# Kernel tuning notes

Hardware: AMD Instinct MI355X
Metric: run time of the kernel (lower is better)

Reference implementation:

```python
import jax, jax.numpy as jnp
import numpy as np

B, T, F = 256, 512, 64
H1, H2, OUT = 100, 128, 19


def setup_inputs() -> dict:
    key = jax.random.key(0)
    ks = jax.random.split(key, 6)
    s = 0.05  # small init so relu cell activation stays stable over 512 steps
    return {
        "x":  jax.random.normal(ks[0], (B, T, F), jnp.float32),
        "W1": jax.random.normal(ks[1], (F, 4 * H1), jnp.float32) * s,
        "U1": jax.random.normal(ks[2], (H1, 4 * H1), jnp.float32) * s,
        "b1": jnp.zeros((4 * H1,), jnp.float32),
        "W2": jax.random.normal(ks[3], (H1, 4 * H2), jnp.float32) * s,
        "U2": jax.random.normal(ks[4], (H2, 4 * H2), jnp.float32) * s,
        "b2": jnp.zeros((4 * H2,), jnp.float32),
        "Wd": jax.random.normal(ks[5], (H2, OUT), jnp.float32) * s,
        "bd": jnp.zeros((OUT,), jnp.float32),
    }


def _lstm_relu(x, W, U, b):
    """Keras LSTM with activation=relu, recurrent_activation=sigmoid.
    x: [B,T,F]. Returns full hidden sequence [B,T,H]. Gate order i,f,g,o."""
    H = U.shape[0]
    xproj = jnp.einsum('btf,fj->btj', x, W) + b  # [B,T,4H], input gemm hoisted out of scan

    def step(carry, xt):
        h, c = carry
        z = xt + h @ U                            # [B,4H]
        i, f, g, o = jnp.split(z, 4, axis=-1)
        i = jax.nn.sigmoid(i)
        f = jax.nn.sigmoid(f)
        g = jax.nn.relu(g)
        o = jax.nn.sigmoid(o)
        c = f * c + i * g
        h = o * jax.nn.relu(c)
        return (h, c), h

    h0 = jnp.zeros((x.shape[0], H), x.dtype)
    c0 = jnp.zeros_like(h0)
    _, hs = jax.lax.scan(step, (h0, c0), jnp.swapaxes(xproj, 0, 1))  # [T,B,H]
    return jnp.swapaxes(hs, 0, 1)


def reference(x, W1, U1, b1, W2, U2, b2, Wd, bd):
    h1 = _lstm_relu(x, W1, U1, b1)    # [B,T,H1] (return_sequences=True, stacked intent)
    h2 = _lstm_relu(h1, W2, U2, b2)   # [B,T,H2]
    last = h2[:, -1]                   # [B,H2] last timestep
    return jax.nn.softmax(last @ Wd + bd, axis=-1)
```

## Files before the change

### kernel.cpp

```cpp
#include <hip/hip_runtime.h>
#include <math.h>

#define B_   256
#define T_   512
#define F_   64
#define H1_  100
#define H2_  128
#define OUT_ 19
#define TCH  64
#define NCH  (T_/TCH)
#define NPC  512
#define KP   128

typedef unsigned int uint;
typedef _Float16 h16;
typedef __attribute__((ext_vector_type(2))) _Float16 h16x2;
typedef __attribute__((ext_vector_type(8))) _Float16 f16x8;
typedef __attribute__((ext_vector_type(4))) float f32x4;

#define XPW_BYTES (16ull*TCH*NPC*16*2)
#define H1G_BYTES (16ull*TCH*KP*16*2)
#define CST_BYTES (16ull*KP*16*4)
#define HST_BYTES (16ull*KP*16*2)
#define UF_BYTES  (128ull*64*8*2)

#define A_XP1A  0ull
#define A_XP1B  (A_XP1A + XPW_BYTES)
#define A_XP2A  (A_XP1B + XPW_BYTES)
#define A_XP2B  (A_XP2A + XPW_BYTES)
#define A_H1GA  (A_XP2B + XPW_BYTES)
#define A_H1GB  (A_H1GA + H1G_BYTES)
#define A_C1    (A_H1GB + H1G_BYTES)
#define A_C2    (A_C1   + CST_BYTES)
#define A_H1S   (A_C2   + CST_BYTES)
#define A_H2S   (A_H1S  + HST_BYTES)
#define A_U1F   (A_H2S  + HST_BYTES)
#define A_U2F   (A_U1F  + UF_BYTES)
#define A_W1F   (A_U2F  + UF_BYTES)
#define A_W2F   (A_W1F  + UF_BYTES)
#define WS_A    (A_W2F  + UF_BYTES)

__device__ __forceinline__ float sigm(float x) { return 1.0f / (1.0f + __expf(-x)); }

__device__ __forceinline__ uint pk2(float a, float b) {
    h16x2 h; h.x = (h16)a; h.y = (h16)b;
    return __builtin_bit_cast(uint, h);
}

__device__ __forceinline__ f32x4 mfma16(f16x8 a, f16x8 b, f32x4 c) {
    return __builtin_amdgcn_mfma_f32_16x16x32_f16(a, b, c, 0, 0, 0);
}

__device__ __forceinline__ f32x4 up4(uint2 v) {
    h16x2 a = __builtin_bit_cast(h16x2, v.x);
    h16x2 b = __builtin_bit_cast(h16x2, v.y);
    f32x4 r; r[0] = (float)a.x; r[1] = (float)a.y; r[2] = (float)b.x; r[3] = (float)b.y;
    return r;
}

__device__ __forceinline__ void bar_lgkm() {
    asm volatile("s_waitcnt lgkmcnt(0)" ::: "memory");
    __builtin_amdgcn_sched_barrier(0);
    __builtin_amdgcn_s_barrier();
    __builtin_amdgcn_sched_barrier(0);
}

__device__ __forceinline__ f16x8 load_bfrag(const float* __restrict__ P, int H, int OG,
                                            int Kreal, int ubase, int g, int q, int lane) {
    const int u  = ubase + (lane & 15);
    const int k0 = q * 32 + (lane >> 4) * 8;
    const int col = g * H + u;
    float f[8];
    #pragma unroll
    for (int e = 0; e < 8; ++e) {
        const int k = k0 + e;
        f[e] = (u < H && k < Kreal) ? P[(size_t)k * OG + col] : 0.0f;
    }
    uint4 r;
    r.x = pk2(f[0], f[1]); r.y = pk2(f[2], f[3]);
    r.z = pk2(f[4], f[5]); r.w = pk2(f[6], f[7]);
    return __builtin_bit_cast(f16x8, r);
}

__global__ __launch_bounds__(512) void k_prepack4(
    const float* __restrict__ U1, const float* __restrict__ U2,
    const float* __restrict__ W1, const float* __restrict__ W2,
    h16* __restrict__ u1f, h16* __restrict__ u2f,
    h16* __restrict__ w1f, h16* __restrict__ w2f)
{
    const int w = blockIdx.x & 7;
    const int which = blockIdx.x >> 3;
    const float* P; int H, K, KF; h16* D;
    if (which == 0)      { P = U1; H = H1_; K = H1_; KF = 4; D = u1f; }
    else if (which == 1) { P = U2; H = H2_; K = H2_; KF = 4; D = u2f; }
    else if (which == 2) { P = W1; H = H1_; K = 64;  KF = 2; D = w1f; }
    else                 { P = W2; H = H2_; K = H1_; KF = 4; D = w2f; }
    const int lane = threadIdx.x & 63;
    #pragma unroll
    for (int it = 0; it < 2; ++it) {
        const int combo = it * 8 + (threadIdx.x >> 6);
        const int g = combo >> 2, q = combo & 3;
        if (q < KF) {
            f16x8 fr = load_bfrag(P, H, 4 * H, K, w * 16, g, q, lane);
            *(f16x8*)(D + (size_t)(((w * 4 + g) * 4 + q) * 64 + lane) * 8) = fr;
        }
    }
}

template<int MODE, int NIT>
__device__ __forceinline__ void dense_body(
    const float* __restrict__ Af, const h16* __restrict__ Ah,
    const h16* __restrict__ Wf, const float* __restrict__ bias,
    const int H, const int ch, h16* __restrict__ xp,
    const int bid, const int j)
{
    const int lane = j & 63, w = j >> 6;
    const int KF = MODE ? 4 : 2;

    f16x8 bf[4][4];
    #pragma unroll
    for (int g = 0; g < 4; ++g)
        #pragma unroll
        for (int q = 0; q < 4; ++q)
            if (q < KF)
                bf[g][q] = *(const f16x8*)(Wf + (size_t)(((w * 4 + g) * 4 + q) * 64 + lane) * 8);

    float bv[4];
    #pragma unroll
    for (int g = 0; g < 4; ++g) {
        const int u = w * 16 + (lane & 15);
        bv[g] = (u < H) ? bias[g * H + u] : 0.0f;
    }

    const int ci = lane & 15, hi = lane >> 4;
    #pragma unroll
    for (int it = 0; it < NIT; ++it) {
        const int m = bid * NIT + it;
        const int bt = m / TCH, tc = m % TCH;

        f16x8 af[4];
        if (MODE == 0) {
            const int b = bt * 16 + ci;
            const int t = ch * TCH + tc;
            #pragma unroll
            for (int q = 0; q < 2; ++q) {
                const int k0 = q * 32 + hi * 8;
                const float* p = Af + ((size_t)b * T_ + t) * F_ + k0;
                float4 x0 = *(const float4*)p;
                float4 x1 = *(const float4*)(p + 4);
                uint4 r;
                r.x = pk2(x0.x, x0.y); r.y = pk2(x0.z, x0.w);
                r.z = pk2(x1.x, x1.y); r.w = pk2(x1.z, x1.w);
                af[q] = __builtin_bit_cast(f16x8, r);
            }
        } else {
            #pragma unroll
            for (int q = 0; q < 4; ++q) {
                const int k0 = q * 32 + hi * 8;
                const size_t base = ((size_t)(bt * TCH + tc) * KP + k0) * 16 + ci;
                f16x8 a;
                #pragma unroll
                for (int e = 0; e < 8; ++e) a[e] = Ah[base + (size_t)e * 16];
                af[q] = a;
            }
        }

        f32x4 acc[4];
        #pragma unroll
        for (int g = 0; g < 4; ++g) { acc[g][0]=bv[g]; acc[g][1]=bv[g]; acc[g][2]=bv[g]; acc[g][3]=bv[g]; }
        #pragma unroll
        for (int g = 0; g < 4; ++g)
            #pragma unroll
            for (int q = 0; q < 4; ++q)
                if (q < KF) acc[g] = mfma16(af[q], bf[g][q], acc[g]);

        #pragma unroll
        for (int g = 0; g < 4; ++g) {
            const int c = (w * 4 + g) * 16 + ci;
            const size_t o = ((size_t)(bt * TCH + tc) * NPC + c) * 16 + hi * 4;
            uint2 s;
            s.x = pk2(acc[g][0], acc[g][1]);
            s.y = pk2(acc[g][2], acc[g][3]);
            *(uint2*)(xp + o) = s;
        }
    }
}

template<int MODE>
__global__ __launch_bounds__(512) void k_dense(
    const float* __restrict__ Af, const h16* __restrict__ Ah,
    const h16* __restrict__ Wf, const float* __restrict__ bias,
    const int H, const int ch, h16* __restrict__ xp)
{
    dense_body<MODE, 4>(Af, Ah, Wf, bias, H, ch, xp, blockIdx.x, threadIdx.x);
}

#define LF(G,Q) f16x8 wf##G##Q = *(const f16x8*)(Uf + (size_t)(((w*4+G)*4+Q)*64 + lane)*8);

#define RSTEP(Pn, tcur)                                                          \
    {                                                                            \
        const int t_ = (tcur);                                                   \
        const h16* hb = &hbuf[t_ & 1][0][0];                                     \
        f16x8 a0 = *(const f16x8*)(hb + ci * 136 + 0  + hi * 8);                 \
        f16x8 a1 = *(const f16x8*)(hb + ci * 136 + 32 + hi * 8);                 \
        f16x8 a2 = *(const f16x8*)(hb + ci * 136 + 64 + hi * 8);                 \
        f16x8 a3 = *(const f16x8*)(hb + ci * 136 + 96 + hi * 8);                 \
        f32x4 z0 = up4(Pn##0), z1 = up4(Pn##1), z2 = up4(Pn##2), z3 = up4(Pn##3);\
        const uint to_ = (uint)((t_ + 2 < TCH) ? t_ + 2 : t_) * xstep;           \
        Pn##0 = *(const uint2*)(xp + xb0 + to_);                                 \
        Pn##1 = *(const uint2*)(xp + xb1 + to_);                                 \
        Pn##2 = *(const uint2*)(xp + xb2 + to_);                                 \
        Pn##3 = *(const uint2*)(xp + xb3 + to_);                                 \
        z0 = mfma16(a0, wf00, z0); z0 = mfma16(a1, wf01, z0);                    \
        z0 = mfma16(a2, wf02, z0); z0 = mfma16(a3, wf03, z0);                    \
        z1 = mfma16(a0, wf10, z1); z1 = mfma16(a1, wf11, z1);                    \
        z1 = mfma16(a2, wf12, z1); z1 = mfma16(a3, wf13, z1);                    \
        z2 = mfma16(a0, wf20, z2); z2 = mfma16(a1, wf21, z2);                    \
        z2 = mfma16(a2, wf22, z2); z2 = mfma16(a3, wf23, z2);                    \
        z3 = mfma16(a0, wf30, z3); z3 = mfma16(a1, wf31, z3);                    \
        z3 = mfma16(a2, wf32, z3); z3 = mfma16(a3, wf33, z3);                    \
        f32x4 hv;                                                                \
        _Pragma("unroll")                                                        \
        for (int i = 0; i < 4; ++i) {                                            \
            float ig = sigm(z0[i]);                                              \
            float fg = sigm(z1[i]);                                              \
            float gg = fmaxf(z2[i], 0.0f);                                       \
            float og = sigm(z3[i]);                                              \
            c[i] = fg * c[i] + ig * gg;                                          \
            hv[i] = og * fmaxf(c[i], 0.0f);                                      \
        }                                                                        \
        h16 h0 = (h16)hv[0], h1 = (h16)hv[1], h2 = (h16)hv[2], h3 = (h16)hv[3]; \
        const int nb_ = (t_ & 1) ^ 1;                                            \
        hbuf[nb_][r0 + 0][myu] = h0;                                             \
        hbuf[nb_][r0 + 1][myu] = h1;                                             \
        hbuf[nb_][r0 + 2][myu] = h2;                                             \
        hbuf[nb_][r0 + 3][myu] = h3;                                             \
        h16x2 p01_; p01_.x = h0; p01_.y = h1;                                    \
        h16x2 p23_; p23_.x = h2; p23_.y = h3;                                    \
        hp.x = __builtin_bit_cast(uint, p01_);                                   \
        hp.y = __builtin_bit_cast(uint, p23_);                                   \
        if (do_hout) *(uint2*)(hout + hob + (uint)t_ * hstep) = hp;              \
        bar_lgkm();                                                              \
    }

__device__ __forceinline__ void rec_body(
    const h16* __restrict__ Uf,
    const h16* __restrict__ xp, h16* __restrict__ hout, const int do_hout,
    float* __restrict__ cstate, h16* __restrict__ hstate, const int ch,
    const int bt, const int j)
{
    __shared__ h16 hbuf[2][16][136];
    const int lane = j & 63, w = j >> 6;
    const int ci = lane & 15, hi = lane >> 4;
    const int myu = w * 16 + ci;
    const int r0 = hi * 4;

    LF(0,0) LF(0,1) LF(0,2) LF(0,3)
    LF(1,0) LF(1,1) LF(1,2) LF(1,3)
    LF(2,0) LF(2,1) LF(2,2) LF(2,3)
    LF(3,0) LF(3,1) LF(3,2) LF(3,3)

    {
        const int u = j & 127, rr = (j >> 7) * 4;
        #pragma unroll
        for (int i = 0; i < 4; ++i) {
            h16 v = (h16)0.0f;
            if (ch != 0) v = hstate[((size_t)bt * KP + u) * 16 + rr + i];
            hbuf[0][rr + i][u] = v;
        }
    }
    f32x4 c;
    const size_t coff = ((size_t)bt * KP + myu) * 16 + r0;
    if (ch == 0) { c[0]=0.f; c[1]=0.f; c[2]=0.f; c[3]=0.f; }
    else         { c = *(const f32x4*)(cstate + coff); }
    __syncthreads();

    const uint xstep = NPC * 16;
    const uint xb0 = (uint)(((size_t)bt * TCH) * NPC + (w * 64 + ci)) * 16 + r0;
    const uint xb1 = xb0 + 16 * 16, xb2 = xb0 + 32 * 16, xb3 = xb0 + 48 * 16;

    uint2 pA0 = *(const uint2*)(xp + xb0);
    uint2 pA1 = *(const uint2*)(xp + xb1);
    uint2 pA2 = *(const uint2*)(xp + xb2);
    uint2 pA3 = *(const uint2*)(xp + xb3);
    uint2 pB0 = *(const uint2*)(xp + xb0 + xstep);
    uint2 pB1 = *(const uint2*)(xp + xb1 + xstep);
    uint2 pB2 = *(const uint2*)(xp + xb2 + xstep);
    uint2 pB3 = *(const uint2*)(xp + xb3 + xstep);

    const uint hstep = KP * 16;
    const uint hob = (uint)(((size_t)bt * TCH) * KP + myu) * 16 + r0;

    uint2 hp; hp.x = 0u; hp.y = 0u;

    for (int tt = 0; tt < TCH; tt += 2) {
        RSTEP(pA, tt)
        RSTEP(pB, tt + 1)
    }

    *(f32x4*)(cstate + coff) = c;
    *(uint2*)(hstate + ((size_t)bt * KP + myu) * 16 + r0) = hp;
}

__global__ __launch_bounds__(512) void k_mega(
    const int rec2_on, const h16* __restrict__ Uf2, const h16* __restrict__ xp2r,
    float* __restrict__ c2, h16* __restrict__ hs2, const int ch2,
    const int rec1_on, const h16* __restrict__ Uf1, const h16* __restrict__ xp1r,
    h16* __restrict__ h1gw, float* __restrict__ c1, h16* __restrict__ hs1, const int ch1,
    const int d2_on, const h16* __restrict__ h1gr, const h16* __restrict__ w2f,
    const float* __restrict__ b2, h16* __restrict__ xp2w,
    const int d1_on, const float* __restrict__ x, const h16* __restrict__ w1f,
    const float* __restrict__ b1, const int chd1, h16* __restrict__ xp1w)
{
    const int bid = blockIdx.x, j = threadIdx.x;
    if (bid < 16) {
        if (rec2_on) rec_body(Uf2, xp2r, (h16*)nullptr, 0, c2, hs2, ch2, bid, j);
    } else if (bid < 32) {
        if (rec1_on) rec_body(Uf1, xp1r, h1gw, 1, c1, hs1, ch1, bid - 16, j);
    } else if (bid < 288) {
        if (d2_on) dense_body<1, 4>((const float*)nullptr, h1gr, w2f, b2, H2_, 0, xp2w, bid - 32, j);
    } else {
        if (d1_on) dense_body<0, 4>(x, (const h16*)nullptr, w1f, b1, H1_, chd1, xp1w, bid - 288, j);
    }
}

__global__ void k_head(const h16* __restrict__ h2s, const float* __restrict__ Wd,
                       const float* __restrict__ bd, float* __restrict__ out)
{
    __shared__ float lg[OUT_];
    const int b = blockIdx.x, j = threadIdx.x;
    const int bt = b >> 4, r = b & 15;
    if (j < OUT_) {
        float acc = bd[j];
        for (int u = 0; u < H2_; ++u)
            acc += (float)h2s[((size_t)bt * KP + u) * 16 + r] * Wd[u * OUT_ + j];
        lg[j] = acc;
    }
    __syncthreads();
    if (j < OUT_) {
        float m = -1e30f;
        for (int k = 0; k < OUT_; ++k) m = fmaxf(m, lg[k]);
        float s = 0.0f;
        for (int k = 0; k < OUT_; ++k) s += expf(lg[k] - m);
        out[b * OUT_ + j] = expf(lg[j] - m) / s;
    }
}

#define G1_  400
#define G2_  512
#define FBTC 32
#define FB_XP1  0
#define FB_XP2  0
#define FB_WQ   51200
#define FB_XS   134400
#define FB_W2Q  32768
#define FB_H1C  139264
#define FB_U2Q  32768
#define FB_ZBUF 160000
#define FB_H1PK 162048
#define FB_H2PK 162256
#define FB_H2F  162512
#define FB_LDS  163328

__device__ __forceinline__ float fd2(uint wv, uint hv, float cc) {
#if __has_builtin(__builtin_amdgcn_fdot2)
    return __builtin_amdgcn_fdot2(__builtin_bit_cast(h16x2, wv),
                                  __builtin_bit_cast(h16x2, hv), cc, false);
#else
    h16x2 a = __builtin_bit_cast(h16x2, wv), b = __builtin_bit_cast(h16x2, hv);
    return cc + (float)a.x * (float)b.x + (float)a.y * (float)b.y;
#endif
}

__device__ __forceinline__ void stage_quads(const float* __restrict__ P, const int G,
                                            const int NQ, const int KREAL,
                                            char* dst, const int j)
{
    if (j < G) {
        for (int q = 0; q < NQ; ++q) {
            float f[8];
            #pragma unroll
            for (int r = 0; r < 8; ++r) {
                const int k = 8 * q + r;
                f[r] = (k < KREAL) ? P[(size_t)k * G + j] : 0.0f;
            }
            uint4 u;
            u.x = pk2(f[0], f[1]); u.y = pk2(f[2], f[3]);
            u.z = pk2(f[4], f[5]); u.w = pk2(f[6], f[7]);
            *(uint4*)(dst + (size_t)(q * G + j) * 16) = u;
        }
    }
}

__global__ __launch_bounds__(512) void lstm_fallback(
    const float* __restrict__ x,
    const float* __restrict__ W1, const float* __restrict__ U1, const float* __restrict__ b1,
    const float* __restrict__ W2, const float* __restrict__ U2, const float* __restrict__ b2,
    const float* __restrict__ Wd, const float* __restrict__ bd,
    float* __restrict__ out)
{
    __shared__ uint4 smem4[FB_LDS / 16];
    char* sm = (char*)smem4;
    const int b = blockIdx.x;
    const int j = threadIdx.x;
    float c1 = 0.0f, c2 = 0.0f;

    const uint u2r0 = pk2(U2[120 * G2_ + j], U2[121 * G2_ + j]);
    const uint u2r1 = pk2(U2[122 * G2_ + j], U2[123 * G2_ + j]);
    const uint u2r2 = pk2(U2[124 * G2_ + j], U2[125 * G2_ + j]);
    const uint u2r3 = pk2(U2[126 * G2_ + j], U2[127 * G2_ + j]);

    if (j < 52) *(uint*)(sm + FB_H1PK + 4 * j) = 0u;
    if (j < 64) *(uint*)(sm + FB_H2PK + 4 * j) = 0u;
    __syncthreads();

    const float* xrow = x + (size_t)b * T_ * F_;
    for (int ch = 0; ch < T_ / FBTC; ++ch) {
        stage_quads(W1, G1_, 8, 64, sm + FB_WQ, j);
        #pragma unroll
        for (int r = 0; r < 2; ++r) {
            int v = r * 512 + j;
            float2 xv = *(const float2*)(xrow + ch * (FBTC * F_) + 2 * v);
            *(uint*)(sm + FB_XS + 4 * v) = pk2(xv.x, xv.y);
        }
        __syncthreads();
        if (j < G1_) {
            const float bj = b1[j];
            const uint4* WQ = (const uint4*)(sm + FB_WQ);
            for (int t = 0; t < FBTC; ++t) {
                const uint4* XQ = (const uint4*)(sm + FB_XS + t * 128);
                float a0 = bj, a1 = 0.f, a2 = 0.f, a3 = 0.f;
                #pragma unroll
                for (int q = 0; q < 8; ++q) {
                    uint4 wq = WQ[q * G1_ + j]; uint4 hq = XQ[q];
                    a0 = fd2(wq.x, hq.x, a0); a1 = fd2(wq.y, hq.y, a1);
                    a2 = fd2(wq.z, hq.z, a2); a3 = fd2(wq.w, hq.w, a3);
                }
                *(float*)(sm + FB_XP1 + 4 * (t * G1_ + j)) = (a0 + a1) + (a2 + a3);
            }
        }
        __syncthreads();
        stage_quads(U1, G1_, 13, H1_, sm + FB_WQ, j);
        __syncthreads();
        for (int t = 0; t < FBTC; ++t) {
            if (j < G1_) {
                const uint4* WQ = (const uint4*)(sm + FB_WQ);
                const uint4* HP = (const uint4*)(sm + FB_H1PK);
                float a0 = *(const float*)(sm + FB_XP1 + 4 * (t * G1_ + j));
                float a1 = 0.f, a2 = 0.f, a3 = 0.f;
                #pragma unroll
                for (int q = 0; q < 13; ++q) {
                    uint4 wq = WQ[q * G1_ + j]; uint4 hq = HP[q];
                    a0 = fd2(wq.x, hq.x, a0); a1 = fd2(wq.y, hq.y, a1);
                    a2 = fd2(wq.z, hq.z, a2); a3 = fd2(wq.w, hq.w, a3);
                }
                *(float*)(sm + FB_ZBUF + 4 * j) = (a0 + a1) + (a2 + a3);
            }
            __syncthreads();
            if (j < H1_) {
                const float* zb = (const float*)(sm + FB_ZBUF);
                float ig = sigm(zb[j]);
                float fg = sigm(zb[H1_ + j]);
                float gg = fmaxf(zb[2 * H1_ + j], 0.0f);
                float og = sigm(zb[3 * H1_ + j]);
                c1 = fg * c1 + ig * gg;
                float h = og * fmaxf(c1, 0.0f);
                h16 hh = (h16)h;
                *(h16*)(sm + FB_H1PK + 2 * j) = hh;
                *(h16*)(sm + FB_H1C + t * 208 + 2 * j) = hh;
            }
            __syncthreads();
        }
        stage_quads(W2, G2_, 13, H1_, sm + FB_W2Q, j);
        __syncthreads();
        {
            const float bj = b2[j];
            const uint4* WQ = (const uint4*)(sm + FB_W2Q);
            for (int t = 0; t < FBTC; ++t) {
                const uint4* HC = (const uint4*)(sm + FB_H1C + t * 208);
                float a0 = bj, a1 = 0.f, a2 = 0.f, a3 = 0.f;
                #pragma unroll
                for (int q = 0; q < 13; ++q) {
                    uint4 wq = WQ[q * G2_ + j]; uint4 hq = HC[q];
                    a0 = fd2(wq.x, hq.x, a0); a1 = fd2(wq.y, hq.y, a1);
                    a2 = fd2(wq.z, hq.z, a2); a3 = fd2(wq.w, hq.w, a3);
                }
                *(h16*)(sm + FB_XP2 + 2 * (t * G2_ + j)) = (h16)((a0 + a1) + (a2 + a3));
            }
        }
        __syncthreads();
        stage_quads(U2, G2_, 15, 120, sm + FB_U2Q, j);
        __syncthreads();
        for (int t = 0; t < FBTC; ++t) {
            {
                const uint4* WQ = (const uint4*)(sm + FB_U2Q);
                const uint4* HP = (const uint4*)(sm + FB_H2PK);
                float a0 = (float)*(const h16*)(sm + FB_XP2 + 2 * (t * G2_ + j));
                float a1 = 0.f, a2 = 0.f, a3 = 0.f;
                #pragma unroll
                for (int q = 0; q < 15; ++q) {
                    uint4 wq = WQ[q * G2_ + j]; uint4 hq = HP[q];
                    a0 = fd2(wq.x, hq.x, a0); a1 = fd2(wq.y, hq.y, a1);
                    a2 = fd2(wq.z, hq.z, a2); a3 = fd2(wq.w, hq.w, a3);
                }
                uint4 hp15 = ((const uint4*)(sm + FB_H2PK))[15];
                a0 = fd2(u2r0, hp15.x, a0); a1 = fd2(u2r1, hp15.y, a1);
                a2 = fd2(u2r2, hp15.z, a2); a3 = fd2(u2r3, hp15.w, a3);
                *(float*)(sm + FB_ZBUF + 4 * j) = (a0 + a1) + (a2 + a3);
            }
            __syncthreads();
            if (j < H2_) {
                const float* zb = (const float*)(sm + FB_ZBUF);
                float ig = sigm(zb[j]);
                float fg = sigm(zb[H2_ + j]);
                float gg = fmaxf(zb[2 * H2_ + j], 0.0f);
                float og = sigm(zb[3 * H2_ + j]);
                c2 = fg * c2 + ig * gg;
                float h = og * fmaxf(c2, 0.0f);
                *(h16*)(sm + FB_H2PK + 2 * j) = (h16)h;
                *(float*)(sm + FB_H2F + 4 * j) = h;
            }
            __syncthreads();
        }
    }
    if (j < OUT_) {
        const float* h2 = (const float*)(sm + FB_H2F);
        float acc = bd[j];
        #pragma unroll
        for (int k = 0; k < H2_; ++k) acc += h2[k] * Wd[k * OUT_ + j];
        *(float*)(sm + FB_ZBUF + 4 * j) = acc;
    }
    __syncthreads();
    if (j < OUT_) {
        const float* zb = (const float*)(sm + FB_ZBUF);
        float m = -1e30f;
        for (int k = 0; k < OUT_; ++k) m = fmaxf(m, zb[k]);
        float s = 0.0f;
        for (int k = 0; k < OUT_; ++k) s += expf(zb[k] - m);
        out[b * OUT_ + j] = expf(zb[j] - m) / s;
    }
}

extern "C" void kernel_launch(void* const* d_in, const int* in_sizes, int n_in,
                              void* d_out, int out_size, void* d_ws, size_t ws_size,
                              hipStream_t stream) {
    const float* x  = (const float*)d_in[0];
    const float* W1 = (const float*)d_in[1];
    const float* U1 = (const float*)d_in[2];
    const float* b1 = (const float*)d_in[3];
    const float* W2 = (const float*)d_in[4];
    const float* U2 = (const float*)d_in[5];
    const float* b2 = (const float*)d_in[6];
    const float* Wd = (const float*)d_in[7];
    const float* bd = (const float*)d_in[8];
    float* out = (float*)d_out;

    if (ws_size >= WS_A) {
        char* ws = (char*)d_ws;
        h16* xp1[2] = { (h16*)(ws + A_XP1A), (h16*)(ws + A_XP1B) };
        h16* xp2[2] = { (h16*)(ws + A_XP2A), (h16*)(ws + A_XP2B) };
        h16* h1g[2] = { (h16*)(ws + A_H1GA), (h16*)(ws + A_H1GB) };
        float* c1  = (float*)(ws + A_C1);
        float* c2  = (float*)(ws + A_C2);
        h16*   hs1 = (h16*)(ws + A_H1S);
        h16*   hs2 = (h16*)(ws + A_H2S);
        h16*   u1f = (h16*)(ws + A_U1F);
        h16*   u2f = (h16*)(ws + A_U2F);
        h16*   w1f = (h16*)(ws + A_W1F);
        h16*   w2f = (h16*)(ws + A_W2F);

        k_prepack4<<<32, 512, 0, stream>>>(U1, U2, W1, W2, u1f, u2f, w1f, w2f);
        k_dense<0><<<256, 512, 0, stream>>>(x, (const h16*)nullptr, w1f, b1, H1_, 0, xp1[0]);
        k_mega<<<544, 512, 0, stream>>>(
            0, u2f, (const h16*)nullptr, c2, hs2, 0,
            1, u1f, xp1[0], h1g[0], c1, hs1, 0,
            0, (const h16*)nullptr, w2f, b2, (h16*)nullptr,
            1, x, w1f, b1, 1, xp1[1]);
        k_mega<<<544, 512, 0, stream>>>(
            0, u2f, (const h16*)nullptr, c2, hs2, 0,
            1, u1f, xp1[1], h1g[1], c1, hs1, 1,
            1, h1g[0], w2f, b2, xp2[0],
            1, x, w1f, b1, 2, xp1[0]);
        for (int ch = 0; ch < NCH; ++ch) {
            const int r1on = (ch + 2 < NCH);
            const int d2on = (ch + 1 < NCH);
            const int d1on = (ch + 3 < NCH);
            k_mega<<<544, 512, 0, stream>>>(
                1, u2f, xp2[ch & 1], c2, hs2, ch,
                r1on, u1f, xp1[(ch + 2) & 1], h1g[(ch + 2) & 1], c1, hs1, ch + 2,
                d2on, h1g[(ch + 1) & 1], w2f, b2, xp2[(ch + 1) & 1],
                d1on, x, w1f, b1, ch + 3, xp1[(ch + 3) & 1]);
        }
        k_head<<<256, 64, 0, stream>>>(hs2, Wd, bd, out);
    } else {
        lstm_fallback<<<B_, 512, 0, stream>>>(x, W1, U1, b1, W2, U2, b2, Wd, bd, out);
    }
}
```

Baseline: 777.4 us.

## Halve time chunk size and fuse weight prepack with first dense projection

```diff
diff --git a/kernel.cpp b/kernel.cpp
--- a/kernel.cpp
+++ b/kernel.cpp
@@ -7,7 +7,7 @@
 #define H1_  100
 #define H2_  128
 #define OUT_ 19
-#define TCH  64
+#define TCH  32
 #define NCH  (T_/TCH)
 #define NPC  512
 #define KP   128
@@ -82,56 +82,21 @@
     return __builtin_bit_cast(f16x8, r);
 }
 
-__global__ __launch_bounds__(512) void k_prepack4(
-    const float* __restrict__ U1, const float* __restrict__ U2,
-    const float* __restrict__ W1, const float* __restrict__ W2,
-    h16* __restrict__ u1f, h16* __restrict__ u2f,
-    h16* __restrict__ w1f, h16* __restrict__ w2f)
-{
-    const int w = blockIdx.x & 7;
-    const int which = blockIdx.x >> 3;
-    const float* P; int H, K, KF; h16* D;
-    if (which == 0)      { P = U1; H = H1_; K = H1_; KF = 4; D = u1f; }
-    else if (which == 1) { P = U2; H = H2_; K = H2_; KF = 4; D = u2f; }
-    else if (which == 2) { P = W1; H = H1_; K = 64;  KF = 2; D = w1f; }
-    else                 { P = W2; H = H2_; K = H1_; KF = 4; D = w2f; }
-    const int lane = threadIdx.x & 63;
-    #pragma unroll
-    for (int it = 0; it < 2; ++it) {
-        const int combo = it * 8 + (threadIdx.x >> 6);
-        const int g = combo >> 2, q = combo & 3;
-        if (q < KF) {
-            f16x8 fr = load_bfrag(P, H, 4 * H, K, w * 16, g, q, lane);
-            *(f16x8*)(D + (size_t)(((w * 4 + g) * 4 + q) * 64 + lane) * 8) = fr;
-        }
-    }
-}
-
 template<int MODE, int NIT>
-__device__ __forceinline__ void dense_body(
+__device__ __forceinline__ void dense_core(
     const float* __restrict__ Af, const h16* __restrict__ Ah,
-    const h16* __restrict__ Wf, const float* __restrict__ bias,
+    const f16x8 bf[4][4], const float* __restrict__ bias,
     const int H, const int ch, h16* __restrict__ xp,
     const int bid, const int j)
 {
     const int lane = j & 63, w = j >> 6;
     const int KF = MODE ? 4 : 2;
-
-    f16x8 bf[4][4];
-    #pragma unroll
-    for (int g = 0; g < 4; ++g)
-        #pragma unroll
-        for (int q = 0; q < 4; ++q)
-            if (q < KF)
-                bf[g][q] = *(const f16x8*)(Wf + (size_t)(((w * 4 + g) * 4 + q) * 64 + lane) * 8);
-
     float bv[4];
     #pragma unroll
     for (int g = 0; g < 4; ++g) {
         const int u = w * 16 + (lane & 15);
         bv[g] = (u < H) ? bias[g * H + u] : 0.0f;
     }
-
     const int ci = lane & 15, hi = lane >> 4;
     #pragma unroll
     for (int it = 0; it < NIT; ++it) {
@@ -186,13 +151,75 @@
     }
 }
 
-template<int MODE>
-__global__ __launch_bounds__(512) void k_dense(
+template<int MODE, int NIT>
+__device__ __forceinline__ void dense_body(
     const float* __restrict__ Af, const h16* __restrict__ Ah,
     const h16* __restrict__ Wf, const float* __restrict__ bias,
-    const int H, const int ch, h16* __restrict__ xp)
-{
-    dense_body<MODE, 4>(Af, Ah, Wf, bias, H, ch, xp, blockIdx.x, threadIdx.x);
+    const int H, const int ch, h16* __restrict__ xp,
+    const int bid, const int j)
+{
+    const int lane = j & 63, w = j >> 6;
+    const int KF = MODE ? 4 : 2;
+    f16x8 bf[4][4];
+    #pragma unroll
+    for (int g = 0; g < 4; ++g)
+        #pragma unroll
+        for (int q = 0; q < 4; ++q)
+            if (q < KF)
+                bf[g][q] = *(const f16x8*)(Wf + (size_t)(((w * 4 + g) * 4 + q) * 64 + lane) * 8);
+    dense_core<MODE, NIT>(Af, Ah, bf, bias, H, ch, xp, bid, j);
+}
+
+template<int MODE, int NIT>
+__device__ __forceinline__ void dense_body_strided(
+    const float* __restrict__ Af, const h16* __restrict__ Ah,
+    const float* __restrict__ W, const float* __restrict__ bias,
+    const int H, const int ch, h16* __restrict__ xp,
+    const int bid, const int j)
+{
+    const int lane = j & 63, w = j >> 6;
+    const int KF = MODE ? 4 : 2;
+    const int KREAL = MODE ? H1_ : 64;
+    f16x8 bf[4][4];
+    #pragma unroll
+    for (int g = 0; g < 4; ++g)
+        #pragma unroll
+        for (int q = 0; q < 4; ++q)
+            if (q < KF) bf[g][q] = load_bfrag(W, H, 4 * H, KREAL, w * 16, g, q, lane);
+    dense_core<MODE, NIT>(Af, Ah, bf, bias, H, ch, xp, bid, j);
+}
+
+__global__ __launch_bounds__(512) void k_prepack_d1(
+    const float* __restrict__ U1, const float* __restrict__ U2,
+    const float* __restrict__ W1, const float* __restrict__ W2,
+    h16* __restrict__ u1f, h16* __restrict__ u2f,
+    h16* __restrict__ w1f, h16* __restrict__ w2f,
+    const float* __restrict__ x, const float* __restrict__ b1,
+    h16* __restrict__ xp1w)
+{
+    const int bid = blockIdx.x;
+    if (bid < 32) {
+        const int w = bid & 7;
+        const int which = bid >> 3;
+        const float* P; int H, K, KF; h16* D;
+        if (which == 0)      { P = U1; H = H1_; K = H1_; KF = 4; D = u1f; }
+        else if (which == 1) { P = U2; H = H2_; K = H2_; KF = 4; D = u2f; }
+        else if (which == 2) { P = W1; H = H1_; K = 64;  KF = 2; D = w1f; }
+        else                 { P = W2; H = H2_; K = H1_; KF = 4; D = w2f; }
+        const int lane = threadIdx.x & 63;
+        #pragma unroll
+        for (int it = 0; it < 2; ++it) {
+            const int combo = it * 8 + (threadIdx.x >> 6);
+            const int g = combo >> 2, q = combo & 3;
+            if (q < KF) {
+                f16x8 fr = load_bfrag(P, H, 4 * H, K, w * 16, g, q, lane);
+                *(f16x8*)(D + (size_t)(((w * 4 + g) * 4 + q) * 64 + lane) * 8) = fr;
+            }
+        }
+    } else {
+        dense_body_strided<0, 2>(x, (const h16*)nullptr, W1, b1, H1_, 0, xp1w,
+                                 bid - 32, threadIdx.x);
+    }
 }
 
 #define LF(G,Q) f16x8 wf##G##Q = *(const f16x8*)(Uf + (size_t)(((w*4+G)*4+Q)*64 + lane)*8);
@@ -316,11 +343,11 @@
     if (bid < 16) {
         if (rec2_on) rec_body(Uf2, xp2r, (h16*)nullptr, 0, c2, hs2, ch2, bid, j);
     } else if (bid < 32) {
-        if (rec1_on) rec_body(Uf1, xp1r, h1gw, 1, c1, hs1, ch1, bid - 16, j);
+        if (rec1_on) rec_body(Uf1, xp1r, h1gw, 1, c1, hs1, bid == 16 ? ch1 : ch1, bid - 16, j);
     } else if (bid < 288) {
-        if (d2_on) dense_body<1, 4>((const float*)nullptr, h1gr, w2f, b2, H2_, 0, xp2w, bid - 32, j);
+        if (d2_on) dense_body<1, 2>((const float*)nullptr, h1gr, w2f, b2, H2_, 0, xp2w, bid - 32, j);
     } else {
-        if (d1_on) dense_body<0, 4>(x, (const h16*)nullptr, w1f, b1, H1_, chd1, xp1w, bid - 288, j);
+        if (d1_on) dense_body<0, 2>(x, (const h16*)nullptr, w1f, b1, H1_, chd1, xp1w, bid - 288, j);
     }
 }
 
@@ -569,8 +596,8 @@
         h16*   w1f = (h16*)(ws + A_W1F);
         h16*   w2f = (h16*)(ws + A_W2F);
 
-        k_prepack4<<<32, 512, 0, stream>>>(U1, U2, W1, W2, u1f, u2f, w1f, w2f);
-        k_dense<0><<<256, 512, 0, stream>>>(x, (const h16*)nullptr, w1f, b1, H1_, 0, xp1[0]);
+        k_prepack_d1<<<288, 512, 0, stream>>>(U1, U2, W1, W2, u1f, u2f, w1f, w2f,
+                                              x, b1, xp1[0]);
         k_mega<<<544, 512, 0, stream>>>(
             0, u2f, (const h16*)nullptr, c2, hs2, 0,
             1, u1f, xp1[0], h1g[0], c1, hs1, 0,
```

After: 748.6 us. -3.7%, faster.
